# Performance work log

Hardware: AMD Instinct MI355X
Metric: run time of the kernel (lower is better)

## Reference

```python
import jax, jax.numpy as jnp
import numpy as np
from jax import lax

SCORE_T = 0.05
NMS_T = 0.5
MAXDET = 300


def batch_iou(b1, b2):
    # b1: [K,4], b2: [K,4] -> [K,K]
    lt = jnp.maximum(b1[:, None, :2], b2[None, :, :2])
    rb = jnp.minimum(b1[:, None, 2:], b2[None, :, 2:])
    inter = jnp.clip(rb - lt, 0.0, None).prod(-1)
    a1 = (b1[:, 2:] - b1[:, :2]).prod(-1)
    a2 = (b2[:, 2:] - b2[:, :2]).prod(-1)
    union = a1[:, None] + a2[None, :] - inter
    return inter / jnp.clip(union, 1e-7, None)


def nms_class(boxes, cls_scores):
    # boxes: [N,4], cls_scores: [N]. Mirrors: score>thresh filter, top-k MAXDET
    # candidates, greedy NMS in descending score order.
    s = jnp.where(cls_scores > SCORE_T, cls_scores, -jnp.inf)
    top_s, idx = lax.top_k(s, MAXDET)          # sorted desc, [K]
    b = jnp.take(boxes, idx, axis=0)            # [K,4]
    v = jnp.isfinite(top_s)                     # passed score threshold
    iou = batch_iou(b, b)                       # [K,K]

    def body(kept, i):
        # keep i iff valid and no already-kept box has IoU >= NMS_T with it
        suppressed = jnp.any(jnp.where(kept, iou[i], 0.0) >= NMS_T)
        return kept.at[i].set(v[i] & ~suppressed), None

    kept, _ = lax.scan(body, jnp.zeros(MAXDET, dtype=bool), jnp.arange(MAXDET))
    return top_s, idx, kept


def per_image(boxes, cls):
    # boxes: [N,4], cls: [N,C]
    C = cls.shape[1]
    top_s, idx, kept = jax.vmap(nms_class, in_axes=(None, 1))(boxes, cls)  # [C,K]
    scores_flat = jnp.where(kept, top_s, -jnp.inf).reshape(-1)  # [C*K]
    idx_flat = idx.reshape(-1)
    labels_flat = jnp.repeat(jnp.arange(C), MAXDET)
    fs, fi = lax.top_k(scores_flat, MAXDET)     # global top-k across classes
    valid = jnp.isfinite(fs)
    box_idx = idx_flat[fi]
    out_boxes = jnp.where(valid[:, None], jnp.take(boxes, box_idx, axis=0), -1.0)
    out_scores = jnp.where(valid, fs, -1.0)
    out_labels = jnp.where(valid, labels_flat[fi], -1).astype(jnp.int32)
    return out_boxes, out_scores, out_labels


def setup_inputs() -> dict:
    key = jax.random.key(0)
    k1, k2, k3 = jax.random.split(key, 3)
    B, N, C = 8, 100000, 80
    centers = jax.random.uniform(k1, (B, N, 2), dtype=jnp.float32) * 1024.0
    wh = jax.random.uniform(k2, (B, N, 2), dtype=jnp.float32) * 96.0 + 4.0
    boxes = jnp.concatenate([centers - wh / 2, centers + wh / 2], axis=-1)
    classification = jax.random.uniform(k3, (B, N, C), dtype=jnp.float32)
    return {"boxes": boxes, "classification": classification}


def reference(boxes, classification):
    # Returns (Boxes [B,MAXDET,4], Scores [B,MAXDET], Labels [B,MAXDET] int32),
    # padded with -1 where fewer than MAXDET detections survive.
    return jax.vmap(per_image)(boxes, classification)
```

## Files before the change

### kernel.cpp

```cpp
#include <hip/hip_runtime.h>

#define BIMG 8
#define NBOX 100000
#define NCLS 80
#define KDET 300
#define CAP  2048
#define CAPC 12
#define TPUSH 0.9921875f
#define SCORE_T 0.05f
#define NELEM 8000000
#define NQ    2000000

typedef unsigned long long u64;
typedef unsigned u32;

#define OFF_PUSHCNT 0u
#define ZERO_BYTES  2560u
#define OFF_BUF     4096u
#define OFF_KCNT    (4096u + 10485760u)
#define OFF_KSC     (OFF_KCNT + 2560u)
#define OFF_KIDX    (OFF_KSC + 768000u)

static __device__ __forceinline__ u64 mk_key(float sc, u32 n) {
  return ((u64)__float_as_uint(sc) << 32) | (u32)(~n);
}

static __device__ __forceinline__ void radix_step(const u32* hist, int nbins,
                                                  int width, u32* sk, u64* spfx,
                                                  u32* ssel) {
  if (threadIdx.x < 64) {
    const int lane = threadIdx.x;
    const int chunk = nbins >> 6;
    u32 psum = 0;
    for (int i = 0; i < chunk; ++i) psum += hist[lane * chunk + i];
    u32 suf = psum;
#pragma unroll
    for (int off = 1; off < 64; off <<= 1) {
      u32 o = __shfl_down(suf, off);
      if (lane + off < 64) suf += o;
    }
    u32 k = *sk;
    u64 bal = __ballot(suf >= k);
    if (bal != 0ull) {
      int L = 63 - __clzll((long long)bal);
      if (lane == L) {
        u32 krem = k - (suf - psum);
        int bi = (L + 1) * chunk - 1;
        u32 acc = 0;
        for (;;) {
          acc += hist[bi];
          if (acc >= krem || bi == L * chunk) break;
          --bi;
        }
        *spfx = (*spfx << width) | (u32)bi;
        *sk = krem - (acc - hist[bi]);
        *ssel = (suf - psum) + acc;
      }
    }
  }
}

__constant__ int RSH[6] = {53, 42, 31, 20, 9, 0};
__constant__ int RWD[6] = {11, 11, 11, 11, 11, 9};

static __device__ __forceinline__ void bitonic512(u64* tk, int t) {
  u64 a = tk[t];
#pragma unroll
  for (int k2 = 2; k2 <= 64; k2 <<= 1) {
#pragma unroll
    for (int j = k2 >> 1; j > 0; j >>= 1) {
      u64 c2 = __shfl_xor(a, j);
      bool takeMax = (((t & k2) == 0) == ((t & j) == 0));
      u64 mx = (a > c2) ? a : c2;
      u64 mn = (a > c2) ? c2 : a;
      a = takeMax ? mx : mn;
    }
  }
#pragma unroll
  for (int k2 = 128; k2 <= 512; k2 <<= 1) {
    for (int j = k2 >> 1; j >= 64; j >>= 1) {
      tk[t] = a;
      __syncthreads();
      u64 c2 = tk[t ^ j];
      bool takeMax = (((t & k2) == 0) == ((t & j) == 0));
      u64 mx = (a > c2) ? a : c2;
      u64 mn = (a > c2) ? c2 : a;
      a = takeMax ? mx : mn;
      __syncthreads();
    }
#pragma unroll
    for (int j = 32; j > 0; j >>= 1) {
      u64 c2 = __shfl_xor(a, j);
      bool takeMax = (((t & k2) == 0) == ((t & j) == 0));
      u64 mx = (a > c2) ? a : c2;
      u64 mn = (a > c2) ? c2 : a;
      a = takeMax ? mx : mn;
    }
  }
  tk[t] = a;
  __syncthreads();
}

static __device__ __forceinline__ void pushone(int c, float sc, u32 n, int b,
                                               u32* lcnt, u64* stage,
                                               u32* pushcnt, u64* buf) {
  u64 key = mk_key(sc, n);
  u32 slot = atomicAdd(&lcnt[c], 1u);
  if (slot < CAPC) {
    stage[c * CAPC + slot] = key;
  } else {
    u32 g = atomicAdd(&pushcnt[b * NCLS + c], 1u);
    if (g < CAP) buf[(size_t)(b * NCLS + c) * CAP + g] = key;
  }
}

__global__ __launch_bounds__(256) void histK(const float* __restrict__ cls,
                                             u32* __restrict__ pushcnt,
                                             u64* __restrict__ buf) {
  __shared__ u32 lcnt[NCLS];
  __shared__ u32 sbase[NCLS];
  __shared__ u64 stage[NCLS * CAPC];

  const int t = threadIdx.x;
  const int b = blockIdx.y;
  for (int i = t; i < NCLS; i += 256) lcnt[i] = 0;
  __syncthreads();

  const float4* base4 = (const float4*)(cls + (size_t)b * NELEM);
  const int start = blockIdx.x * 8192;

#define PROCQ(u) do { \
    float mx = fmaxf(fmaxf(v##u.x, v##u.y), fmaxf(v##u.z, v##u.w)); \
    if (mx >= TPUSH) { \
      const int e0 = q##u * 4; \
      const int c0 = e0 % NCLS; \
      const u32 n = (u32)(e0 / NCLS); \
      if (v##u.x >= TPUSH) pushone(c0 + 0, v##u.x, n, b, lcnt, stage, pushcnt, buf); \
      if (v##u.y >= TPUSH) pushone(c0 + 1, v##u.y, n, b, lcnt, stage, pushcnt, buf); \
      if (v##u.z >= TPUSH) pushone(c0 + 2, v##u.z, n, b, lcnt, stage, pushcnt, buf); \
      if (v##u.w >= TPUSH) pushone(c0 + 3, v##u.w, n, b, lcnt, stage, pushcnt, buf); \
    } } while (0)

  if (start + 8192 <= NQ) {
    for (int it = 0; it < 4; ++it) {
      const int qb = start + it * 2048 + t;
#define LOADF(u) const int q##u = qb + (u) * 256; const float4 v##u = base4[q##u]
      LOADF(0); LOADF(1); LOADF(2); LOADF(3);
      LOADF(4); LOADF(5); LOADF(6); LOADF(7);
#undef LOADF
      PROCQ(0); PROCQ(1); PROCQ(2); PROCQ(3);
      PROCQ(4); PROCQ(5); PROCQ(6); PROCQ(7);
    }
  } else {
    for (int it = 0; it < 4; ++it) {
      const int qb = start + it * 2048 + t;
#define LOADC(u) const int q##u = qb + (u) * 256; \
  const float4 v##u = (q##u < NQ) ? base4[q##u] : make_float4(0.f, 0.f, 0.f, 0.f)
      LOADC(0); LOADC(1); LOADC(2); LOADC(3);
      LOADC(4); LOADC(5); LOADC(6); LOADC(7);
#undef LOADC
      PROCQ(0); PROCQ(1); PROCQ(2); PROCQ(3);
      PROCQ(4); PROCQ(5); PROCQ(6); PROCQ(7);
    }
  }
#undef PROCQ
  __syncthreads();

  if (t < NCLS) {
    u32 cnt = min(lcnt[t], (u32)CAPC);
    sbase[t] = cnt ? atomicAdd(&pushcnt[b * NCLS + t], cnt) : 0u;
  }
  __syncthreads();
  for (int idx = t; idx < NCLS * CAPC; idx += 256) {
    const int c = idx / CAPC;
    const int k = idx - c * CAPC;
    if ((u32)k < min(lcnt[c], (u32)CAPC)) {
      u32 s = sbase[c] + (u32)k;
      if (s < CAP) buf[(size_t)(b * NCLS + c) * CAP + s] = stage[idx];
    }
  }
}

__global__ __launch_bounds__(512) void nmsK(const float* __restrict__ boxes,
                                            const float* __restrict__ cls,
                                            const u32* __restrict__ pushcnt,
                                            u64* __restrict__ buf,
                                            u32* __restrict__ keptCnt,
                                            float* __restrict__ keptScore,
                                            u32* __restrict__ keptIdx) {
  __shared__ float bx[KDET][4];
  __shared__ float scl[KDET];
  __shared__ u32 nn_[KDET];
  __shared__ u64 msk[KDET][5];
  __shared__ u64 tk[512];
  __shared__ u64 keptw[5];
  __shared__ u64 spfx;
  __shared__ u64 sand, sor;
  __shared__ u32 sk, ssel, stcnt;
  __shared__ u32 sfpfx, sfk, sfab, sfeq, sfmode, sfbcnt;

  const int t = threadIdx.x;
  const int bc = blockIdx.x;
  const int b = bc / NCLS;
  u64* bufp = buf + (size_t)bc * CAP;
  u32* hist = (u32*)&msk[0][0];

  if (t == 0) { spfx = 0ull; sk = KDET; stcnt = 0u; sfmode = 0u; sfbcnt = 0u; }

  u32 realcnt = pushcnt[bc];
  const bool dofb = !(realcnt >= (u32)KDET && realcnt <= (u32)CAP);
  if (dofb) {
    const int c = bc % NCLS;
    const float* col = cls + (size_t)b * NELEM + c;
    for (int r = 0; r < 3; ++r) {
      const int shift = (r == 0) ? 21 : (r == 1) ? 10 : 0;
      const int nbins = (r == 2) ? 1024 : 2048;
      for (int i = t; i < nbins; i += 512) hist[i] = 0;
      __syncthreads();
      for (int n = t; n < NBOX; n += 512) {
        float sc = col[(size_t)n * NCLS];
        if (sc > SCORE_T) {
          u32 u = __float_as_uint(sc);
          bool ok = (r == 0) || (r == 1 ? ((u >> 21) == (sfpfx >> 21))
                                        : ((u >> 10) == (sfpfx >> 10)));
          if (ok) atomicAdd(&hist[(u >> shift) & (u32)(nbins - 1)], 1u);
        }
      }
      __syncthreads();
      if (t == 0) {
        if (r == 0) {
          u32 s = 0;
          for (int i = 0; i < nbins; ++i) s += hist[i];
          if (s < KDET) sfmode = 1u;
        }
        if (sfmode == 0u) {
          u32 kk2 = (r == 0) ? (u32)KDET : sfk;
          u32 acc = 0;
          int bi = nbins - 1;
          for (; bi >= 0; --bi) {
            if (acc + hist[bi] >= kk2) break;
            acc += hist[bi];
          }
          sfk = kk2 - acc;
          sfpfx = ((r == 0) ? 0u : sfpfx) | ((u32)bi << shift);
          if (r == 2) { sfeq = hist[bi]; sfab = KDET - sfk; }
        }
      }
      __syncthreads();
      if (sfmode == 1u) break;
    }

    if (sfmode == 1u) {
      for (int n = t; n < NBOX; n += 512) {
        float sc = col[(size_t)n * NCLS];
        if (sc > SCORE_T) {
          u32 g = atomicAdd(&sfbcnt, 1u);
          if (g < CAP) bufp[g] = mk_key(sc, (u32)n);
        }
      }
    } else {
      const u32 ustar = sfpfx;
      const u32 m = sfab, e = sfeq;
      if (m + e <= CAP) {
        for (int n = t; n < NBOX; n += 512) {
          float sc = col[(size_t)n * NCLS];
          if (sc > SCORE_T && __float_as_uint(sc) >= ustar) {
            u32 g = atomicAdd(&sfbcnt, 1u);
            if (g < CAP) bufp[g] = mk_key(sc, (u32)n);
          }
        }
      } else {
        for (int n = t; n < NBOX; n += 512) {
          float sc = col[(size_t)n * NCLS];
          if (sc > SCORE_T && __float_as_uint(sc) > ustar) {
            u32 g = atomicAdd(&sfbcnt, 1u);
            if (g < CAP) bufp[g] = mk_key(sc, (u32)n);
          }
        }
        __syncthreads();
        if (t == 0) {
          u32 room = CAP - m, got = 0;
          for (int n = 0; n < NBOX && got < room; ++n) {
            float sc = col[(size_t)n * NCLS];
            if (sc > SCORE_T && __float_as_uint(sc) == ustar) {
              u32 g = atomicAdd(&sfbcnt, 1u);
              if (g < CAP) bufp[g] = mk_key(sc, (u32)n);
              ++got;
            }
          }
        }
      }
    }
    __threadfence_block();
    __syncthreads();
    realcnt = sfbcnt;
  }
  const int cnt = min((int)realcnt, CAP);

  u64 kk[4];
#pragma unroll
  for (int u = 0; u < 4; ++u) {
    int i = t + u * 512;
    u64 v = 0ull;
    if (i < cnt)
      v = dofb ? *((volatile const u64*)(bufp + i)) : bufp[i];
    kk[u] = v;
  }

  const bool normal = (cnt > KDET);
  int eshift = 0;
  u64 ethr = 1ull;
  if (normal) {
    if (t == 0) { sand = ~0ull; sor = 0ull; }
    __syncthreads();
    {
      u64 ka = ~0ull, ko = 0ull;
#pragma unroll
      for (int u = 0; u < 4; ++u) {
        u64 key = kk[u];
        if (key) { ka &= key; ko |= key; }
      }
#pragma unroll
      for (int off = 32; off > 0; off >>= 1) {
        ka &= __shfl_xor(ka, off);
        ko |= __shfl_xor(ko, off);
      }
      if ((t & 63) == 0) {
        atomicAnd((unsigned long long*)&sand, (unsigned long long)ka);
        atomicOr((unsigned long long*)&sor, (unsigned long long)ko);
      }
    }
    __syncthreads();
    const u64 kand = sand, kor = sor;
    for (int p = 0; p < 6; ++p) {
      const int nb = (p == 5) ? 512 : 2048;
      const u32 mask = (u32)(nb - 1);
      const u32 ba = (u32)(kand >> RSH[p]) & mask;
      const u32 bo = (u32)(kor >> RSH[p]) & mask;
      if (ba == bo) {
        if (t == 0) spfx = (spfx << RWD[p]) | (u64)ba;
        __syncthreads();
        continue;
      }
      for (int i = t; i < nb; i += 512) hist[i] = 0;
      __syncthreads();
      const u64 pfx = spfx;
      const u32 skPrev = sk;
#pragma unroll
      for (int u = 0; u < 4; ++u) {
        u64 key = kk[u];
        if (!key) continue;
        if (p > 0 && (key >> RSH[p - 1]) != pfx) continue;
        atomicAdd(&hist[(u32)(key >> RSH[p]) & mask], 1u);
      }
      __syncthreads();
      radix_step(hist, nb, RWD[p], &sk, &spfx, &ssel);
      __syncthreads();
      if ((u32)KDET - skPrev + ssel <= 512u) { eshift = RSH[p]; break; }
    }
    ethr = spfx;
  }

  tk[t] = 0ull;
  __syncthreads();
  {
    const int lane = t & 63;
    const u64 lmlt = (1ull << lane) - 1ull;
#pragma unroll
    for (int u = 0; u < 4; ++u) {
      u64 key = kk[u];
      bool q = (key != 0ull) && ((key >> eshift) >= ethr);
      u64 bal = __ballot(q);
      u32 nw = (u32)__popcll(bal);
      if (nw) {
        u32 base = 0;
        if (lane == 0) base = atomicAdd(&stcnt, nw);
        base = __shfl(base, 0);
        if (q) {
          u32 pos = base + (u32)__popcll(bal & lmlt);
          if (pos < 512) tk[pos] = key;
        }
      }
    }
  }
  __syncthreads();

  bitonic512(tk, t);

  const int M = min((int)stcnt, KDET);
  for (int i = t; i < M; i += 512) {
    u64 key = tk[i];
    u32 n = ~(u32)key;
    scl[i] = __uint_as_float((u32)(key >> 32));
    nn_[i] = n;
    const float4 bv = *(const float4*)(boxes + ((size_t)b * NBOX + n) * 4);
    bx[i][0] = bv.x; bx[i][1] = bv.y; bx[i][2] = bv.z; bx[i][3] = bv.w;
  }
  __syncthreads();

  for (int tau = t; tau < KDET * 5; tau += 512) {
    const int i = tau / 5;
    const int w = tau - i * 5;
    u64 m = 0ull;
    const int jb = w << 6;
    if (i < M && jb < i) {
      const int je = min(i, jb + 64);
      const float x1 = bx[i][0], y1 = bx[i][1], x2 = bx[i][2], y2 = bx[i][3];
      const float a1 = (x2 - x1) * (y2 - y1);
      for (int j = jb; j < je; ++j) {
        float lx = fmaxf(x1, bx[j][0]);
        float ly = fmaxf(y1, bx[j][1]);
        float rx = fminf(x2, bx[j][2]);
        float ry = fminf(y2, bx[j][3]);
        float iw = fmaxf(rx - lx, 0.0f), ih = fmaxf(ry - ly, 0.0f);
        float inter = iw * ih;
        float a2 = (bx[j][2] - bx[j][0]) * (bx[j][3] - bx[j][1]);
        float uni = fmaxf(a1 + a2 - inter, 1e-7f);
        float iou = inter / uni;
        if (iou >= 0.5f) m |= 1ull << (j & 63);
      }
    }
    if (i < M) msk[i][w] = m;
  }
  __syncthreads();

  if (t < 64) {
    u64 kwv[5];
#pragma unroll
    for (int w = 0; w < 5; ++w) {
      const int i = w * 64 + t;
      bool pb = (i < M);
      u64 mown = 0ull;
      if (pb) {
#pragma unroll
        for (int w2 = 0; w2 < 5; ++w2)
          if (w2 < w && (msk[i][w2] & kwv[w2])) pb = false;
        mown = msk[i][w];
      }
      u64 kv = 0ull;
      for (;;) {
        u64 bal = __ballot(pb && ((mown & kv) == 0ull));
        if (!bal) break;
        int p = __ffsll((unsigned long long)bal) - 1;
        kv |= 1ull << p;
        if (t == p) pb = false;
      }
      kwv[w] = kv;
      if (t == 0) keptw[w] = kv;
    }
  }
  __syncthreads();

  for (int i = t; i < M; i += 512) {
    if ((keptw[i >> 6] >> (i & 63)) & 1ull) {
      int rank = 0;
      for (int w = 0; w < (i >> 6); ++w) rank += __popcll(keptw[w]);
      rank += __popcll(keptw[i >> 6] & ((1ull << (i & 63)) - 1ull));
      keptScore[(size_t)bc * KDET + rank] = scl[i];
      keptIdx[(size_t)bc * KDET + rank] = nn_[i];
    }
  }
  if (t == 0) {
    int tot = 0;
    for (int w = 0; w < 5; ++w) tot += __popcll(keptw[w]);
    keptCnt[bc] = (u32)tot;
  }
}

__global__ __launch_bounds__(512) void mergeK(const float* __restrict__ boxes,
                                              const u32* __restrict__ keptCnt,
                                              const float* __restrict__ keptScore,
                                              const u32* __restrict__ keptIdx,
                                              float* __restrict__ out) {
  __shared__ u32 hist[2048];
  __shared__ int msc[NCLS];
  __shared__ u64 tk[512];
  __shared__ u64 spfx, sand, sor;
  __shared__ u32 sk, ssel, stcnt, smtot;

  const int t = threadIdx.x;
  const int b = blockIdx.x;
  if (t < NCLS) msc[t] = min((int)keptCnt[b * NCLS + t], KDET);
  if (t == 0) {
    spfx = 0ull; sk = KDET; stcnt = 0u; smtot = 0u; sand = ~0ull; sor = 0ull;
  }
  __syncthreads();

  const float* ksc = keptScore + (size_t)b * NCLS * KDET;
#define MKEY(idx, key) do { \
    int c_ = (idx) / KDET, r_ = (idx) - c_ * KDET; \
    key = (r_ < msc[c_]) ? ((u64)__float_as_uint(ksc[idx]) << 32) | (u32)(~(u32)(idx)) \
                         : 0ull; \
  } while (0)

  {
    u64 ka = ~0ull, ko = 0ull;
    u32 mycnt = 0;
    for (int idx = t; idx < NCLS * KDET; idx += 512) {
      u64 key; MKEY(idx, key);
      if (key) { ka &= key; ko |= key; ++mycnt; }
    }
#pragma unroll
    for (int off = 32; off > 0; off >>= 1) {
      ka &= __shfl_xor(ka, off);
      ko |= __shfl_xor(ko, off);
      mycnt += __shfl_xor(mycnt, off);
    }
    if ((t & 63) == 0) {
      atomicAnd((unsigned long long*)&sand, (unsigned long long)ka);
      atomicOr((unsigned long long*)&sor, (unsigned long long)ko);
      atomicAdd(&smtot, mycnt);
    }
  }
  __syncthreads();

  const bool mnormal = ((int)smtot > KDET);
  int eshift = 0;
  u64 ethr = 1ull;
  if (mnormal) {
    const u64 kand = sand, kor = sor;
    for (int p = 0; p < 6; ++p) {
      const int nb = (p == 5) ? 512 : 2048;
      const u32 mask = (u32)(nb - 1);
      const u32 ba = (u32)(kand >> RSH[p]) & mask;
      const u32 bo = (u32)(kor >> RSH[p]) & mask;
      if (ba == bo) {
        if (t == 0) spfx = (spfx << RWD[p]) | (u64)ba;
        __syncthreads();
        continue;
      }
      for (int i = t; i < nb; i += 512) hist[i] = 0;
      __syncthreads();
      const u64 pfx = spfx;
      const u32 skPrev = sk;
      for (int idx = t; idx < NCLS * KDET; idx += 512) {
        u64 key; MKEY(idx, key);
        if (!key) continue;
        if (p > 0 && (key >> RSH[p - 1]) != pfx) continue;
        atomicAdd(&hist[(u32)(key >> RSH[p]) & mask], 1u);
      }
      __syncthreads();
      radix_step(hist, nb, RWD[p], &sk, &spfx, &ssel);
      __syncthreads();
      if ((u32)KDET - skPrev + ssel <= 512u) { eshift = RSH[p]; break; }
    }
    ethr = spfx;
  }

  tk[t] = 0ull;
  __syncthreads();
  {
    const int lane = t & 63;
    const u64 lmlt = (1ull << lane) - 1ull;
    for (int i0 = 0; i0 < NCLS * KDET; i0 += 512) {
      const int idx = i0 + t;
      u64 key = 0ull;
      if (idx < NCLS * KDET) MKEY(idx, key);
      bool q = (key != 0ull) && ((key >> eshift) >= ethr);
      u64 bal = __ballot(q);
      u32 nw = (u32)__popcll(bal);
      if (nw) {
        u32 base = 0;
        if (lane == 0) base = atomicAdd(&stcnt, nw);
        base = __shfl(base, 0);
        if (q) {
          u32 pos = base + (u32)__popcll(bal & lmlt);
          if (pos < 512) tk[pos] = key;
        }
      }
    }
  }
  __syncthreads();
#undef MKEY

  bitonic512(tk, t);

  if (t < KDET) {
    float* ob = out + ((size_t)b * KDET + t) * 4;
    float* os = out + (size_t)BIMG * KDET * 4;
    float* ol = os + (size_t)BIMG * KDET;
    u64 key = tk[t];
    if (key == 0ull) {
      *(float4*)ob = make_float4(-1.f, -1.f, -1.f, -1.f);
      os[(size_t)b * KDET + t] = -1.f;
      ol[(size_t)b * KDET + t] = -1.f;
    } else {
      u32 fi = ~(u32)key;
      int c = fi / KDET, r = fi - c * KDET;
      u32 n = keptIdx[((size_t)b * NCLS + c) * KDET + r];
      *(float4*)ob = *(const float4*)(boxes + ((size_t)b * NBOX + n) * 4);
      os[(size_t)b * KDET + t] = __uint_as_float((u32)(key >> 32));
      ol[(size_t)b * KDET + t] = (float)c;
    }
  }
}

extern "C" void kernel_launch(void* const* d_in, const int* in_sizes, int n_in,
                              void* d_out, int out_size, void* d_ws, size_t ws_size,
                              hipStream_t stream) {
  const float* boxes = (const float*)d_in[0];
  const float* cls = (const float*)d_in[1];
  float* out = (float*)d_out;
  char* ws = (char*)d_ws;

  u32* pushcnt = (u32*)(ws + OFF_PUSHCNT);
  u64* buf = (u64*)(ws + OFF_BUF);
  u32* keptCnt = (u32*)(ws + OFF_KCNT);
  float* keptScore = (float*)(ws + OFF_KSC);
  u32* keptIdx = (u32*)(ws + OFF_KIDX);

  (void)hipMemsetAsync(ws + OFF_PUSHCNT, 0, ZERO_BYTES, stream);

  histK<<<dim3(245, BIMG), 256, 0, stream>>>(cls, pushcnt, buf);
  nmsK<<<BIMG * NCLS, 512, 0, stream>>>(boxes, cls, pushcnt, buf, keptCnt,
                                        keptScore, keptIdx);
  mergeK<<<BIMG, 512, 0, stream>>>(boxes, keptCnt, keptScore, keptIdx, out);
}
```

Measured before the change: 523.0 us.

## Replace bitonic sort with rank-by-counting and start radix select at top differing digit

Replaces the 512-element bitonic sort (with many block barriers) with a rank-by-counting scatter, where each thread counts how many staged keys exceed its own and writes directly to that rank. The radix select now starts at the highest 11-bit digit where the keys differ and steps down uniformly, which removes the constant-table per-pass logic. The shared box array is padded to five floats per row to reduce bank conflicts. The counting rank is O(n) shared reads per thread but avoids roughly two dozen syncthreads per sort; it relies on keys being unique, which holds because the index is embedded in each key.

```diff
diff --git a/kernel.cpp b/kernel.cpp
--- a/kernel.cpp
+++ b/kernel.cpp
@@ -25,12 +25,15 @@
   return ((u64)__float_as_uint(sc) << 32) | (u32)(~n);
 }
 
-static __device__ __forceinline__ void radix_step(const u32* hist, int nbins,
-                                                  int width, u32* sk, u64* spfx,
-                                                  u32* ssel) {
+static __device__ __forceinline__ u64 shr64(u64 v, int s) {
+  return (s >= 64) ? 0ull : (v >> s);
+}
+
+static __device__ __forceinline__ void radix_step(const u32* hist, u32* sk,
+                                                  u64* spfx, u32* ssel) {
   if (threadIdx.x < 64) {
     const int lane = threadIdx.x;
-    const int chunk = nbins >> 6;
+    const int chunk = 32;
     u32 psum = 0;
     for (int i = 0; i < chunk; ++i) psum += hist[lane * chunk + i];
     u32 suf = psum;
@@ -52,53 +55,12 @@
           if (acc >= krem || bi == L * chunk) break;
           --bi;
         }
-        *spfx = (*spfx << width) | (u32)bi;
+        *spfx = (*spfx << 11) | (u32)bi;
         *sk = krem - (acc - hist[bi]);
         *ssel = (suf - psum) + acc;
       }
     }
   }
-}
-
-__constant__ int RSH[6] = {53, 42, 31, 20, 9, 0};
-__constant__ int RWD[6] = {11, 11, 11, 11, 11, 9};
-
-static __device__ __forceinline__ void bitonic512(u64* tk, int t) {
-  u64 a = tk[t];
-#pragma unroll
-  for (int k2 = 2; k2 <= 64; k2 <<= 1) {
-#pragma unroll
-    for (int j = k2 >> 1; j > 0; j >>= 1) {
-      u64 c2 = __shfl_xor(a, j);
-      bool takeMax = (((t & k2) == 0) == ((t & j) == 0));
-      u64 mx = (a > c2) ? a : c2;
-      u64 mn = (a > c2) ? c2 : a;
-      a = takeMax ? mx : mn;
-    }
-  }
-#pragma unroll
-  for (int k2 = 128; k2 <= 512; k2 <<= 1) {
-    for (int j = k2 >> 1; j >= 64; j >>= 1) {
-      tk[t] = a;
-      __syncthreads();
-      u64 c2 = tk[t ^ j];
-      bool takeMax = (((t & k2) == 0) == ((t & j) == 0));
-      u64 mx = (a > c2) ? a : c2;
-      u64 mn = (a > c2) ? c2 : a;
-      a = takeMax ? mx : mn;
-      __syncthreads();
-    }
-#pragma unroll
-    for (int j = 32; j > 0; j >>= 1) {
-      u64 c2 = __shfl_xor(a, j);
-      bool takeMax = (((t & k2) == 0) == ((t & j) == 0));
-      u64 mx = (a > c2) ? a : c2;
-      u64 mn = (a > c2) ? c2 : a;
-      a = takeMax ? mx : mn;
-    }
-  }
-  tk[t] = a;
-  __syncthreads();
 }
 
 static __device__ __forceinline__ void pushone(int c, float sc, u32 n, int b,
@@ -188,7 +150,7 @@
                                             u32* __restrict__ keptCnt,
                                             float* __restrict__ keptScore,
                                             u32* __restrict__ keptIdx) {
-  __shared__ float bx[KDET][4];
+  __shared__ float bx[KDET][5];
   __shared__ float scl[KDET];
   __shared__ u32 nn_[KDET];
   __shared__ u64 msk[KDET][5];
@@ -332,33 +294,31 @@
     }
     __syncthreads();
     const u64 kand = sand, kor = sor;
-    for (int p = 0; p < 6; ++p) {
-      const int nb = (p == 5) ? 512 : 2048;
-      const u32 mask = (u32)(nb - 1);
-      const u32 ba = (u32)(kand >> RSH[p]) & mask;
-      const u32 bo = (u32)(kor >> RSH[p]) & mask;
-      if (ba == bo) {
-        if (t == 0) spfx = (spfx << RWD[p]) | (u64)ba;
-        __syncthreads();
-        continue;
-      }
-      for (int i = t; i < nb; i += 512) hist[i] = 0;
-      __syncthreads();
-      const u64 pfx = spfx;
+    const u64 W = kand ^ kor;
+    const int hv = 63 - __clzll((long long)W);
+    int s = 11 * (hv / 11);
+    if (t == 0) spfx = shr64(kand, s + 11);
+    for (;;) {
+      for (int i = t; i < 2048; i += 512) hist[i] = 0;
+      __syncthreads();
+      const u64 pfxHi = spfx;
       const u32 skPrev = sk;
 #pragma unroll
       for (int u = 0; u < 4; ++u) {
         u64 key = kk[u];
         if (!key) continue;
-        if (p > 0 && (key >> RSH[p - 1]) != pfx) continue;
-        atomicAdd(&hist[(u32)(key >> RSH[p]) & mask], 1u);
-      }
-      __syncthreads();
-      radix_step(hist, nb, RWD[p], &sk, &spfx, &ssel);
-      __syncthreads();
-      if ((u32)KDET - skPrev + ssel <= 512u) { eshift = RSH[p]; break; }
+        if (shr64(key, s + 11) != pfxHi) continue;
+        atomicAdd(&hist[(u32)(key >> s) & 2047u], 1u);
+      }
+      __syncthreads();
+      radix_step(hist, &sk, &spfx, &ssel);
+      __syncthreads();
+      if ((u32)KDET - skPrev + ssel <= 512u || s == 0) { eshift = s; break; }
+      s -= 11;
     }
     ethr = spfx;
+  } else {
+    __syncthreads();
   }
 
   tk[t] = 0ull;
@@ -369,7 +329,7 @@
 #pragma unroll
     for (int u = 0; u < 4; ++u) {
       u64 key = kk[u];
-      bool q = (key != 0ull) && ((key >> eshift) >= ethr);
+      bool q = (key != 0ull) && (shr64(key, eshift) >= ethr);
       u64 bal = __ballot(q);
       u32 nw = (u32)__popcll(bal);
       if (nw) {
@@ -385,16 +345,23 @@
   }
   __syncthreads();
 
-  bitonic512(tk, t);
-
-  const int M = min((int)stcnt, KDET);
-  for (int i = t; i < M; i += 512) {
-    u64 key = tk[i];
-    u32 n = ~(u32)key;
-    scl[i] = __uint_as_float((u32)(key >> 32));
-    nn_[i] = n;
-    const float4 bv = *(const float4*)(boxes + ((size_t)b * NBOX + n) * 4);
-    bx[i][0] = bv.x; bx[i][1] = bv.y; bx[i][2] = bv.z; bx[i][3] = bv.w;
+  const int sc = min((int)stcnt, 512);
+  const int M = min(sc, KDET);
+  {
+    const u64 mykey = tk[t];
+    const int scU = (sc + 7) & ~7;
+    int rank = 0;
+    for (int j = 0; j < scU; j += 8) {
+#pragma unroll
+      for (int jj = 0; jj < 8; ++jj) rank += (tk[j + jj] > mykey) ? 1 : 0;
+    }
+    if (mykey != 0ull && rank < KDET) {
+      u32 n = ~(u32)mykey;
+      scl[rank] = __uint_as_float((u32)(mykey >> 32));
+      nn_[rank] = n;
+      const float4 bv = *(const float4*)(boxes + ((size_t)b * NBOX + n) * 4);
+      bx[rank][0] = bv.x; bx[rank][1] = bv.y; bx[rank][2] = bv.z; bx[rank][3] = bv.w;
+    }
   }
   __syncthreads();
 
@@ -519,30 +486,26 @@
   u64 ethr = 1ull;
   if (mnormal) {
     const u64 kand = sand, kor = sor;
-    for (int p = 0; p < 6; ++p) {
-      const int nb = (p == 5) ? 512 : 2048;
-      const u32 mask = (u32)(nb - 1);
-      const u32 ba = (u32)(kand >> RSH[p]) & mask;
-      const u32 bo = (u32)(kor >> RSH[p]) & mask;
-      if (ba == bo) {
-        if (t == 0) spfx = (spfx << RWD[p]) | (u64)ba;
-        __syncthreads();
-        continue;
-      }
-      for (int i = t; i < nb; i += 512) hist[i] = 0;
-      __syncthreads();
-      const u64 pfx = spfx;
+    const u64 W = kand ^ kor;
+    const int hv = 63 - __clzll((long long)W);
+    int s = 11 * (hv / 11);
+    if (t == 0) spfx = shr64(kand, s + 11);
+    for (;;) {
+      for (int i = t; i < 2048; i += 512) hist[i] = 0;
+      __syncthreads();
+      const u64 pfxHi = spfx;
       const u32 skPrev = sk;
       for (int idx = t; idx < NCLS * KDET; idx += 512) {
         u64 key; MKEY(idx, key);
         if (!key) continue;
-        if (p > 0 && (key >> RSH[p - 1]) != pfx) continue;
-        atomicAdd(&hist[(u32)(key >> RSH[p]) & mask], 1u);
-      }
-      __syncthreads();
-      radix_step(hist, nb, RWD[p], &sk, &spfx, &ssel);
-      __syncthreads();
-      if ((u32)KDET - skPrev + ssel <= 512u) { eshift = RSH[p]; break; }
+        if (shr64(key, s + 11) != pfxHi) continue;
+        atomicAdd(&hist[(u32)(key >> s) & 2047u], 1u);
+      }
+      __syncthreads();
+      radix_step(hist, &sk, &spfx, &ssel);
+      __syncthreads();
+      if ((u32)KDET - skPrev + ssel <= 512u || s == 0) { eshift = s; break; }
+      s -= 11;
     }
     ethr = spfx;
   }
@@ -556,7 +519,7 @@
       const int idx = i0 + t;
       u64 key = 0ull;
       if (idx < NCLS * KDET) MKEY(idx, key);
-      bool q = (key != 0ull) && ((key >> eshift) >= ethr);
+      bool q = (key != 0ull) && (shr64(key, eshift) >= ethr);
       u64 bal = __ballot(q);
       u32 nw = (u32)__popcll(bal);
       if (nw) {
@@ -573,7 +536,21 @@
   __syncthreads();
 #undef MKEY
 
-  bitonic512(tk, t);
+  const int sc = min((int)stcnt, 512);
+  {
+    const u64 mykey = tk[t];
+    const int scU = (sc + 7) & ~7;
+    int rank = 0;
+    for (int j = 0; j < scU; j += 8) {
+#pragma unroll
+      for (int jj = 0; jj < 8; ++jj) rank += (tk[j + jj] > mykey) ? 1 : 0;
+    }
+    __syncthreads();
+    tk[t] = 0ull;
+    __syncthreads();
+    if (mykey != 0ull && rank < KDET) tk[rank] = mykey;
+  }
+  __syncthreads();
 
   if (t < KDET) {
     float* ob = out + ((size_t)b * KDET + t) * 4;
```

Result: no change. 520.3 us (-0.5%).
